# Optimization experiments

Measured on AMD Instinct MI355X. Metric: run time of the kernel, lower is better.

## Reference

```python
import jax, jax.numpy as jnp
import numpy as np

N = 50000   # nodes
E = 640000  # edges
D = 128     # feature dim (din == dmid, required since edge_attr is reused every layer)
L = 5       # GINEConv layers
BN_EPS = 1e-5


def setup_inputs() -> dict:
    key = jax.random.key(0)
    ks = jax.random.split(key, 8)
    x = jax.random.normal(ks[0], (N, D), dtype=jnp.float32)
    edge_index = jax.random.randint(ks[1], (2, E), 0, N, dtype=jnp.int64)
    edge_attr = jax.random.normal(ks[2], (E, D), dtype=jnp.float32)
    W1 = jax.random.normal(ks[3], (L, D, D), dtype=jnp.float32) * 0.05
    b1 = jnp.zeros((L, D), dtype=jnp.float32)
    gamma = jnp.ones((L, D), dtype=jnp.float32)
    beta = jnp.zeros((L, D), dtype=jnp.float32)
    W2 = jax.random.normal(ks[4], (L, D, D), dtype=jnp.float32) * 0.05
    b2 = jnp.zeros((L, D), dtype=jnp.float32)
    return {"x": x, "edge_index": edge_index, "edge_attr": edge_attr,
            "W1": W1, "b1": b1, "gamma": gamma, "beta": beta, "W2": W2, "b2": b2}


def reference(x, edge_index, edge_attr, W1, b1, gamma, beta, W2, b2):
    src, dst = edge_index[0], edge_index[1]  # PyG: messages flow src(j) -> dst(i)
    h = x
    for l in range(L):
        # GINEConv message + aggregate: sum_j ReLU(x_j + e_ij)
        m = jax.nn.relu(h[src] + edge_attr)               # [E, D] gather + add
        agg = jax.ops.segment_sum(m, dst, num_segments=N)  # [N, D] scatter-sum
        h = agg + h  # (1 + eps) * x_i with eps = 0
        # MLP: Linear -> BatchNorm1d (batch stats) -> ReLU -> Linear
        h = h @ W1[l] + b1[l]
        mu = jnp.mean(h, axis=0)
        var = jnp.var(h, axis=0)  # biased var, as torch BN uses for normalization
        h = gamma[l] * (h - mu) * jax.lax.rsqrt(var + BN_EPS) + beta[l]
        h = jax.nn.relu(h)
        h = h @ W2[l] + b2[l]
    return h
```

## Files before the change

kernel.cpp:

```cpp
#include <hip/hip_runtime.h>
#include <hip/hip_bf16.h>
#include <stdint.h>

#define D 128
#define LAYERS 5
#define BN_EPS 1e-5f

typedef unsigned int uint32;
typedef __bf16 bf16x8 __attribute__((ext_vector_type(8)));
typedef float f32x4 __attribute__((ext_vector_type(4)));
typedef float f32x2 __attribute__((ext_vector_type(2)));

__device__ inline unsigned short f2bf(float f) {
    uint32 u = __float_as_uint(f);
    return (unsigned short)((u + 0x7fffu + ((u >> 16) & 1u)) >> 16);
}
__device__ inline float bflo(uint32 p) { return __uint_as_float(p << 16); }
__device__ inline float bfhi(uint32 p) { return __uint_as_float(p & 0xffff0000u); }
__device__ inline uint32 pack2(float a, float b) {
    return (uint32)f2bf(a) | ((uint32)f2bf(b) << 16);
}


__global__ void detect_kernel(const int* __restrict__ ei, int* __restrict__ flag) {
    if (threadIdx.x == 0 && blockIdx.x == 0) {
        int allz = 1;
#pragma unroll
        for (int i = 0; i < 16; ++i) allz &= (ei[2 * i + 1] == 0);
        *flag = allz;
    }
}


__global__ __launch_bounds__(256) void hist_kernel(const int* __restrict__ ei,
                                                   const int* __restrict__ flag,
                                                   int* __restrict__ deg, int E, int n) {
    int e = blockIdx.x * blockDim.x + threadIdx.x;
    if (e >= E) return;
    int is64 = *flag;
    int d = is64 ? ei[2 * ((size_t)E + e)] : ei[E + e];
    if ((unsigned)d < (unsigned)n) atomicAdd(&deg[d], 1);
}

__global__ __launch_bounds__(1024) void scan_kernel(const int* __restrict__ deg,
                                                    int* __restrict__ off, int n) {
    __shared__ int tsum[1024];
    int t = threadIdx.x;
    int CH = (n + 1023) >> 10;
    int lo = t * CH;
    int hi = lo + CH; if (hi > n) hi = n;
    int s = 0;
    for (int i = lo; i < hi; ++i) s += deg[i];
    tsum[t] = s;
    __syncthreads();
    for (int d = 1; d < 1024; d <<= 1) {
        int v = (t >= d) ? tsum[t - d] : 0;
        __syncthreads();
        tsum[t] += v;
        __syncthreads();
    }
    int run = tsum[t] - s;
    for (int i = lo; i < hi; ++i) { off[i] = run; run += deg[i]; }
    if (t == 1023) off[n] = tsum[1023];
}

__global__ __launch_bounds__(256) void fill_kernel(const int* __restrict__ ei,
                                                   const int* __restrict__ flag,
                                                   const int* __restrict__ off,
                                                   int* __restrict__ cursor,
                                                   int* __restrict__ srcs,
                                                   int* __restrict__ eidx, int E, int n) {
    int e = blockIdx.x * blockDim.x + threadIdx.x;
    if (e >= E) return;
    int is64 = *flag;
    int d = is64 ? ei[2 * ((size_t)E + e)] : ei[E + e];
    int s = is64 ? ei[2 * (size_t)e] : ei[e];
    if ((unsigned)d >= (unsigned)n || (unsigned)s >= (unsigned)n) return;
    int p = atomicAdd(&cursor[d], 1);
    int pos = off[d] + p;
    srcs[pos] = s;
    eidx[pos] = e;
}


__global__ __launch_bounds__(256) void wt_kernel(const float* __restrict__ W1,
                                                 const float* __restrict__ W2,
                                                 unsigned short* __restrict__ wt) {
    int id = blockIdx.x * 256 + threadIdx.x;
    if (id >= 10 * 16384) return;
    int l = id >> 14;
    int rem = id & 16383;
    int nn = rem >> 7, kk = rem & 127;
    const float* base = (l < 5) ? (W1 + (size_t)l * 16384) : (W2 + (size_t)(l - 5) * 16384);
    wt[(size_t)l * 16384 + nn * 128 + kk] = f2bf(base[kk * 128 + nn]);
}


__global__ __launch_bounds__(256) void xb_kernel(const float* __restrict__ x,
                                                 uint32* __restrict__ xb, int total) {
    int i = blockIdx.x * 256 + threadIdx.x;
    if (i >= total) return;
    f32x2 v = *(const f32x2*)(x + 2 * (size_t)i);
    xb[i] = pack2(v.x, v.y);
}


__global__ __launch_bounds__(256) void cvt_kernel(const float* __restrict__ ea,
                                                  const int* __restrict__ eidx,
                                                  uint32* __restrict__ eab, int E) {
    int wid = ((blockIdx.x * 256 + threadIdx.x) >> 6) * 2;
    int lane = threadIdx.x & 63;
    if (wid >= E) return;
    int y0 = eidx[wid];
    f32x2 v0 = __builtin_nontemporal_load((const f32x2*)(ea + (size_t)y0 * D + lane * 2));
    if (wid + 1 < E) {
        int y1 = eidx[wid + 1];
        f32x2 v1 = __builtin_nontemporal_load((const f32x2*)(ea + (size_t)y1 * D + lane * 2));
        __builtin_nontemporal_store(pack2(v0.x, v0.y), eab + (size_t)wid * 64 + lane);
        __builtin_nontemporal_store(pack2(v1.x, v1.y), eab + (size_t)(wid + 1) * 64 + lane);
    } else {
        __builtin_nontemporal_store(pack2(v0.x, v0.y), eab + (size_t)wid * 64 + lane);
    }
}


__global__ __launch_bounds__(256) void agg_kernel(const uint32* __restrict__ h,
                                                  const uint32* __restrict__ eab,
                                                  const int* __restrict__ off,
                                                  const int* __restrict__ srcs,
                                                  uint32* __restrict__ out, int n) {
    int node = blockIdx.x * 4 + (threadIdx.x >> 6);
    if (node >= n) return;
    int lane = threadIdx.x & 63;
    uint32 hn = h[(size_t)node * 64 + lane];
    float2 acc = make_float2(bflo(hn), bfhi(hn));
    int e = off[node], end = off[node + 1];
    for (; e + 4 <= end; e += 4) {
        int s0 = srcs[e], s1 = srcs[e + 1], s2 = srcs[e + 2], s3 = srcs[e + 3];
        uint32 a0 = __builtin_nontemporal_load(eab + (size_t)e * 64 + lane);
        uint32 a1 = __builtin_nontemporal_load(eab + (size_t)(e + 1) * 64 + lane);
        uint32 a2 = __builtin_nontemporal_load(eab + (size_t)(e + 2) * 64 + lane);
        uint32 a3 = __builtin_nontemporal_load(eab + (size_t)(e + 3) * 64 + lane);
        uint32 h0 = h[(size_t)s0 * 64 + lane];
        uint32 h1 = h[(size_t)s1 * 64 + lane];
        uint32 h2 = h[(size_t)s2 * 64 + lane];
        uint32 h3 = h[(size_t)s3 * 64 + lane];
        acc.x += fmaxf(bflo(h0) + bflo(a0), 0.f) + fmaxf(bflo(h1) + bflo(a1), 0.f)
               + fmaxf(bflo(h2) + bflo(a2), 0.f) + fmaxf(bflo(h3) + bflo(a3), 0.f);
        acc.y += fmaxf(bfhi(h0) + bfhi(a0), 0.f) + fmaxf(bfhi(h1) + bfhi(a1), 0.f)
               + fmaxf(bfhi(h2) + bfhi(a2), 0.f) + fmaxf(bfhi(h3) + bfhi(a3), 0.f);
    }
    for (; e < end; ++e) {
        int s0 = srcs[e];
        uint32 a0 = eab[(size_t)e * 64 + lane];
        uint32 h0 = h[(size_t)s0 * 64 + lane];
        acc.x += fmaxf(bflo(h0) + bflo(a0), 0.f);
        acc.y += fmaxf(bfhi(h0) + bfhi(a0), 0.f);
    }
    out[(size_t)node * 64 + lane] = pack2(acc.x, acc.y);
}


template <int MODE, bool F32OUT>
__global__ __launch_bounds__(256) void gemm_kernel(const uint4* __restrict__ A,
                                                   const uint4* __restrict__ Wt4,
                                                   const float* __restrict__ bias,
                                                   void* __restrict__ outp,
                                                   float* __restrict__ colstats,
                                                   const float* __restrict__ gamma,
                                                   const float* __restrict__ beta,
                                                   float inv_n, int n) {
    __shared__ float red[256];
    const int t = threadIdx.x;
    const int wv = t >> 6, l = t & 63;
    const int lrow = l & 15, lk = l >> 4;
    const int r0 = blockIdx.x * 64 + wv * 16;

    if (MODE == 1) {
        red[t] = 0.f;
    } else {
        if (t < 128) {
            float mu = colstats[t] * inv_n;
            float var = colstats[128 + t] * inv_n - mu * mu;
            float inv = rsqrtf(var + BN_EPS);
            float sc = gamma[t] * inv;
            red[t] = sc;
            red[128 + t] = beta[t] - mu * sc;
        }
    }
    __syncthreads();

    bf16x8 af[4];
    const int arow = r0 + lrow;
    const bool rowok = arow < n;
#pragma unroll
    for (int c = 0; c < 4; ++c) {
        union { uint4 u; bf16x8 v; uint32 w[4]; } bu;
        bu.u = make_uint4(0u, 0u, 0u, 0u);
        if (rowok) bu.u = A[(size_t)arow * 16 + c * 4 + lk];
        if (MODE == 2) {
            const int kb = c * 32 + lk * 8;
            float xv[8];
#pragma unroll
            for (int i = 0; i < 4; ++i) {
                xv[2 * i]     = bflo(bu.w[i]);
                xv[2 * i + 1] = bfhi(bu.w[i]);
            }
#pragma unroll
            for (int j = 0; j < 8; ++j)
                xv[j] = fmaxf(fmaf(red[kb + j], xv[j], red[128 + kb + j]), 0.f);
#pragma unroll
            for (int i = 0; i < 4; ++i)
                bu.w[i] = pack2(xv[2 * i], xv[2 * i + 1]);
        }
        af[c] = bu.v;
    }

    float* outF = (float*)outp;
    unsigned short* outB = (unsigned short*)outp;
    float s[8], s2[8];

#pragma unroll
    for (int n0 = 0; n0 < 8; ++n0) {
        const int wcol = n0 * 16 + lrow;
        f32x4 acc = {0.f, 0.f, 0.f, 0.f};
#pragma unroll
        for (int c = 0; c < 4; ++c) {
            union { uint4 u; bf16x8 v; } bu;
            bu.u = Wt4[wcol * 16 + c * 4 + lk];
            acc = __builtin_amdgcn_mfma_f32_16x16x32_bf16(af[c], bu.v, acc, 0, 0, 0);
        }
        const float bcol = bias[wcol];
        float ls = 0.f, ls2 = 0.f;
#pragma unroll
        for (int r = 0; r < 4; ++r) {
            int row = r0 + lk * 4 + r;
            float v = acc[r] + bcol;
            if (row < n) {
                if (F32OUT) outF[(size_t)row * D + wcol] = v;
                else        outB[(size_t)row * D + wcol] = f2bf(v);
                if (MODE == 1) { ls += v; ls2 += v * v; }
            }
        }
        s[n0] = ls; s2[n0] = ls2;
    }

    if (MODE == 1) {
#pragma unroll
        for (int n0 = 0; n0 < 8; ++n0) {
            const int wcol = n0 * 16 + lrow;
            float ls = s[n0], ls2 = s2[n0];
            ls  += __shfl_xor(ls, 16);  ls  += __shfl_xor(ls, 32);
            ls2 += __shfl_xor(ls2, 16); ls2 += __shfl_xor(ls2, 32);
            if (lk == 0) {
                atomicAdd(&red[wcol], ls);
                atomicAdd(&red[D + wcol], ls2);
            }
        }
        __syncthreads();
        if (t < 128) {
            atomicAdd(&colstats[t], red[t]);
            atomicAdd(&colstats[D + t], red[D + t]);
        }
    }
}


extern "C" void kernel_launch(void* const* d_in, const int* in_sizes, int n_in,
                              void* d_out, int out_size, void* d_ws, size_t ws_size,
                              hipStream_t stream) {
    const float* x      = (const float*)d_in[0];
    const int*   ei     = (const int*)d_in[1];
    const float* ea     = (const float*)d_in[2];
    const float* W1     = (const float*)d_in[3];
    const float* b1     = (const float*)d_in[4];
    const float* gamma  = (const float*)d_in[5];
    const float* beta   = (const float*)d_in[6];
    const float* W2     = (const float*)d_in[7];
    const float* b2     = (const float*)d_in[8];
    const int N = in_sizes[0] / D;
    const int E = in_sizes[1] / 2;

    char* w = (char*)d_ws;
    auto alloc = [&](size_t bytes) {
        char* p = w;
        w += (bytes + 255) & ~(size_t)255;
        return p;
    };
    int*    off      = (int*)alloc((size_t)(N + 1) * sizeof(int));
    int*    zbase    = (int*)alloc(((size_t)2 * N + 5 * 256) * sizeof(int));
    int*    deg      = zbase;
    int*    cursor   = zbase + N;
    float*  colstats = (float*)(zbase + 2 * N);
    int*    flag     = (int*)alloc(256);
    unsigned short* wt = (unsigned short*)alloc(10 * 16384 * sizeof(unsigned short));
    int*    srcs     = (int*)alloc((size_t)E * sizeof(int));
    int*    eidx     = (int*)alloc((size_t)E * sizeof(int));
    uint32* eab      = (uint32*)alloc((size_t)E * 64 * sizeof(uint32));
    uint32* xb       = (uint32*)alloc((size_t)N * 64 * sizeof(uint32));
    uint32* G        = (uint32*)alloc((size_t)N * 64 * sizeof(uint32));
    uint32* T        = (uint32*)alloc((size_t)N * 64 * sizeof(uint32));
    uint32* H        = (uint32*)alloc((size_t)N * 64 * sizeof(uint32));

    wt_kernel<<<(10 * 16384 + 255) / 256, 256, 0, stream>>>(W1, W2, wt);
    detect_kernel<<<1, 64, 0, stream>>>(ei, flag);
    hipMemsetAsync(zbase, 0, ((size_t)2 * N + 5 * 256) * sizeof(int), stream);
    hist_kernel<<<(E + 255) / 256, 256, 0, stream>>>(ei, flag, deg, E, N);
    scan_kernel<<<1, 1024, 0, stream>>>(deg, off, N);
    fill_kernel<<<(E + 255) / 256, 256, 0, stream>>>(ei, flag, off, cursor, srcs, eidx, E, N);
    xb_kernel<<<(N * 64 + 255) / 256, 256, 0, stream>>>(x, xb, N * 64);
    cvt_kernel<<<(E + 7) / 8, 256, 0, stream>>>(ea, eidx, eab, E);

    const int gemmBlocks = (N + 63) / 64;
    const int aggBlocks  = (N + 3) / 4;
    const float inv_n = 1.0f / (float)N;

    const uint32* hin = xb;
    for (int l = 0; l < LAYERS; ++l) {
        float* cst = colstats + l * 256;
        const uint4* wt1 = (const uint4*)(wt + (size_t)l * 16384);
        const uint4* wt2 = (const uint4*)(wt + (size_t)(5 + l) * 16384);
        agg_kernel<<<aggBlocks, 256, 0, stream>>>(hin, eab, off, srcs, G, N);
        gemm_kernel<1, false><<<gemmBlocks, 256, 0, stream>>>(
            (const uint4*)G, wt1, b1 + l * D, T, cst, nullptr, nullptr, inv_n, N);
        if (l < LAYERS - 1)
            gemm_kernel<2, false><<<gemmBlocks, 256, 0, stream>>>(
                (const uint4*)T, wt2, b2 + l * D, H, cst,
                gamma + l * D, beta + l * D, inv_n, N);
        else
            gemm_kernel<2, true><<<gemmBlocks, 256, 0, stream>>>(
                (const uint4*)T, wt2, b2 + l * D, d_out, cst,
                gamma + l * D, beta + l * D, inv_n, N);
        hin = H;
    }
}
```

Measured before the change: 849.3 us.

## Fuse edge-attr conversion into first-layer aggregation and vectorize gather loads

New measurement: 782.8 us. 1.08x faster.

```diff
diff --git a/kernel.cpp b/kernel.cpp
--- a/kernel.cpp
+++ b/kernel.cpp
@@ -10,6 +10,8 @@
 typedef __bf16 bf16x8 __attribute__((ext_vector_type(8)));
 typedef float f32x4 __attribute__((ext_vector_type(4)));
 typedef float f32x2 __attribute__((ext_vector_type(2)));
+typedef uint32 u32x2 __attribute__((ext_vector_type(2)));
+typedef uint32 u32x4 __attribute__((ext_vector_type(4)));
 
 __device__ inline unsigned short f2bf(float f) {
     uint32 u = __float_as_uint(f);
@@ -96,30 +98,54 @@
 }
 
 
-__global__ __launch_bounds__(256) void xb_kernel(const float* __restrict__ x,
-                                                 uint32* __restrict__ xb, int total) {
-    int i = blockIdx.x * 256 + threadIdx.x;
-    if (i >= total) return;
-    f32x2 v = *(const f32x2*)(x + 2 * (size_t)i);
-    xb[i] = pack2(v.x, v.y);
-}
-
-
-__global__ __launch_bounds__(256) void cvt_kernel(const float* __restrict__ ea,
-                                                  const int* __restrict__ eidx,
-                                                  uint32* __restrict__ eab, int E) {
-    int wid = ((blockIdx.x * 256 + threadIdx.x) >> 6) * 2;
-    int lane = threadIdx.x & 63;
-    if (wid >= E) return;
-    int y0 = eidx[wid];
-    f32x2 v0 = __builtin_nontemporal_load((const f32x2*)(ea + (size_t)y0 * D + lane * 2));
-    if (wid + 1 < E) {
-        int y1 = eidx[wid + 1];
-        f32x2 v1 = __builtin_nontemporal_load((const f32x2*)(ea + (size_t)y1 * D + lane * 2));
-        __builtin_nontemporal_store(pack2(v0.x, v0.y), eab + (size_t)wid * 64 + lane);
-        __builtin_nontemporal_store(pack2(v1.x, v1.y), eab + (size_t)(wid + 1) * 64 + lane);
-    } else {
-        __builtin_nontemporal_store(pack2(v0.x, v0.y), eab + (size_t)wid * 64 + lane);
+__global__ __launch_bounds__(256) void agg_cvt_kernel(const float* __restrict__ x,
+                                                      const float* __restrict__ ea,
+                                                      const int* __restrict__ off,
+                                                      const int* __restrict__ srcs,
+                                                      const int* __restrict__ eidx,
+                                                      uint32* __restrict__ eab,
+                                                      uint32* __restrict__ out, int n) {
+    int node = blockIdx.x * 4 + (threadIdx.x >> 6);
+    if (node >= n) return;
+    const int lane = threadIdx.x & 63;
+    const int half = lane >> 5;
+    const int q = lane & 31;
+    f32x4 acc = {0.f, 0.f, 0.f, 0.f};
+    int e = off[node], end = off[node + 1];
+    for (; e + 4 <= end; e += 4) {
+        int eA = e + half, eB = e + 2 + half;
+        int sA = srcs[eA], sB = srcs[eB];
+        int yA = eidx[eA], yB = eidx[eB];
+        f32x4 va = __builtin_nontemporal_load((const f32x4*)(ea + (size_t)yA * D + q * 4));
+        f32x4 vb = __builtin_nontemporal_load((const f32x4*)(ea + (size_t)yB * D + q * 4));
+        f32x4 ha = *(const f32x4*)(x + (size_t)sA * D + q * 4);
+        f32x4 hb = *(const f32x4*)(x + (size_t)sB * D + q * 4);
+#pragma unroll
+        for (int k = 0; k < 4; ++k)
+            acc[k] += fmaxf(ha[k] + va[k], 0.f) + fmaxf(hb[k] + vb[k], 0.f);
+        u32x2 pa = {pack2(va[0], va[1]), pack2(va[2], va[3])};
+        u32x2 pb = {pack2(vb[0], vb[1]), pack2(vb[2], vb[3])};
+        __builtin_nontemporal_store(pa, (u32x2*)(eab + (size_t)eA * 64 + q * 2));
+        __builtin_nontemporal_store(pb, (u32x2*)(eab + (size_t)eB * 64 + q * 2));
+    }
+    for (; e < end; ++e) {
+        if (half == 0) {
+            int s0 = srcs[e], y0 = eidx[e];
+            f32x4 v = __builtin_nontemporal_load((const f32x4*)(ea + (size_t)y0 * D + q * 4));
+            f32x4 h = *(const f32x4*)(x + (size_t)s0 * D + q * 4);
+#pragma unroll
+            for (int k = 0; k < 4; ++k) acc[k] += fmaxf(h[k] + v[k], 0.f);
+            u32x2 pv = {pack2(v[0], v[1]), pack2(v[2], v[3])};
+            __builtin_nontemporal_store(pv, (u32x2*)(eab + (size_t)e * 64 + q * 2));
+        }
+    }
+#pragma unroll
+    for (int k = 0; k < 4; ++k) acc[k] += __shfl_xor(acc[k], 32);
+    if (half == 0) {
+        f32x4 xs = *(const f32x4*)(x + (size_t)node * D + q * 4);
+        u32x2 o = {pack2(xs[0] + acc[0], xs[1] + acc[1]),
+                   pack2(xs[2] + acc[2], xs[3] + acc[3])};
+        *(u32x2*)(out + (size_t)node * 64 + q * 2) = o;
     }
 }
 
@@ -131,33 +157,63 @@
                                                   uint32* __restrict__ out, int n) {
     int node = blockIdx.x * 4 + (threadIdx.x >> 6);
     if (node >= n) return;
-    int lane = threadIdx.x & 63;
-    uint32 hn = h[(size_t)node * 64 + lane];
-    float2 acc = make_float2(bflo(hn), bfhi(hn));
+    const int lane = threadIdx.x & 63;
+    const int g = lane >> 4;
+    const int j = lane & 15;
+    float acc[8] = {0.f, 0.f, 0.f, 0.f, 0.f, 0.f, 0.f, 0.f};
     int e = off[node], end = off[node + 1];
-    for (; e + 4 <= end; e += 4) {
-        int s0 = srcs[e], s1 = srcs[e + 1], s2 = srcs[e + 2], s3 = srcs[e + 3];
-        uint32 a0 = __builtin_nontemporal_load(eab + (size_t)e * 64 + lane);
-        uint32 a1 = __builtin_nontemporal_load(eab + (size_t)(e + 1) * 64 + lane);
-        uint32 a2 = __builtin_nontemporal_load(eab + (size_t)(e + 2) * 64 + lane);
-        uint32 a3 = __builtin_nontemporal_load(eab + (size_t)(e + 3) * 64 + lane);
-        uint32 h0 = h[(size_t)s0 * 64 + lane];
-        uint32 h1 = h[(size_t)s1 * 64 + lane];
-        uint32 h2 = h[(size_t)s2 * 64 + lane];
-        uint32 h3 = h[(size_t)s3 * 64 + lane];
-        acc.x += fmaxf(bflo(h0) + bflo(a0), 0.f) + fmaxf(bflo(h1) + bflo(a1), 0.f)
-               + fmaxf(bflo(h2) + bflo(a2), 0.f) + fmaxf(bflo(h3) + bflo(a3), 0.f);
-        acc.y += fmaxf(bfhi(h0) + bfhi(a0), 0.f) + fmaxf(bfhi(h1) + bfhi(a1), 0.f)
-               + fmaxf(bfhi(h2) + bfhi(a2), 0.f) + fmaxf(bfhi(h3) + bfhi(a3), 0.f);
+    for (; e + 8 <= end; e += 8) {
+        int e0 = e + g, e1 = e + 4 + g;
+        int s0 = srcs[e0], s1 = srcs[e1];
+        u32x4 a0 = __builtin_nontemporal_load((const u32x4*)(eab + (size_t)e0 * 64 + j * 4));
+        u32x4 a1 = __builtin_nontemporal_load((const u32x4*)(eab + (size_t)e1 * 64 + j * 4));
+        u32x4 h0 = *(const u32x4*)(h + (size_t)s0 * 64 + j * 4);
+        u32x4 h1 = *(const u32x4*)(h + (size_t)s1 * 64 + j * 4);
+#pragma unroll
+        for (int k = 0; k < 4; ++k) {
+            acc[2 * k]     += fmaxf(bflo(h0[k]) + bflo(a0[k]), 0.f)
+                            + fmaxf(bflo(h1[k]) + bflo(a1[k]), 0.f);
+            acc[2 * k + 1] += fmaxf(bfhi(h0[k]) + bfhi(a0[k]), 0.f)
+                            + fmaxf(bfhi(h1[k]) + bfhi(a1[k]), 0.f);
+        }
+    }
+    if (e + 4 <= end) {
+        int e0 = e + g;
+        int s0 = srcs[e0];
+        u32x4 a0 = __builtin_nontemporal_load((const u32x4*)(eab + (size_t)e0 * 64 + j * 4));
+        u32x4 h0 = *(const u32x4*)(h + (size_t)s0 * 64 + j * 4);
+#pragma unroll
+        for (int k = 0; k < 4; ++k) {
+            acc[2 * k]     += fmaxf(bflo(h0[k]) + bflo(a0[k]), 0.f);
+            acc[2 * k + 1] += fmaxf(bfhi(h0[k]) + bfhi(a0[k]), 0.f);
+        }
+        e += 4;
     }
     for (; e < end; ++e) {
-        int s0 = srcs[e];
-        uint32 a0 = eab[(size_t)e * 64 + lane];
-        uint32 h0 = h[(size_t)s0 * 64 + lane];
-        acc.x += fmaxf(bflo(h0) + bflo(a0), 0.f);
-        acc.y += fmaxf(bfhi(h0) + bfhi(a0), 0.f);
-    }
-    out[(size_t)node * 64 + lane] = pack2(acc.x, acc.y);
+        if (g == 0) {
+            int s0 = srcs[e];
+            u32x4 a0 = *(const u32x4*)(eab + (size_t)e * 64 + j * 4);
+            u32x4 h0 = *(const u32x4*)(h + (size_t)s0 * 64 + j * 4);
+#pragma unroll
+            for (int k = 0; k < 4; ++k) {
+                acc[2 * k]     += fmaxf(bflo(h0[k]) + bflo(a0[k]), 0.f);
+                acc[2 * k + 1] += fmaxf(bfhi(h0[k]) + bfhi(a0[k]), 0.f);
+            }
+        }
+    }
+#pragma unroll
+    for (int k = 0; k < 8; ++k) {
+        acc[k] += __shfl_xor(acc[k], 16);
+        acc[k] += __shfl_xor(acc[k], 32);
+    }
+    if (g == 0) {
+        u32x4 hn = *(const u32x4*)(h + (size_t)node * 64 + j * 4);
+        u32x4 o;
+#pragma unroll
+        for (int k = 0; k < 4; ++k)
+            o[k] = pack2(bflo(hn[k]) + acc[2 * k], bfhi(hn[k]) + acc[2 * k + 1]);
+        *(u32x4*)(out + (size_t)node * 64 + j * 4) = o;
+    }
 }
 
 
@@ -297,7 +353,6 @@
     int*    srcs     = (int*)alloc((size_t)E * sizeof(int));
     int*    eidx     = (int*)alloc((size_t)E * sizeof(int));
     uint32* eab      = (uint32*)alloc((size_t)E * 64 * sizeof(uint32));
-    uint32* xb       = (uint32*)alloc((size_t)N * 64 * sizeof(uint32));
     uint32* G        = (uint32*)alloc((size_t)N * 64 * sizeof(uint32));
     uint32* T        = (uint32*)alloc((size_t)N * 64 * sizeof(uint32));
     uint32* H        = (uint32*)alloc((size_t)N * 64 * sizeof(uint32));
@@ -308,19 +363,20 @@
     hist_kernel<<<(E + 255) / 256, 256, 0, stream>>>(ei, flag, deg, E, N);
     scan_kernel<<<1, 1024, 0, stream>>>(deg, off, N);
     fill_kernel<<<(E + 255) / 256, 256, 0, stream>>>(ei, flag, off, cursor, srcs, eidx, E, N);
-    xb_kernel<<<(N * 64 + 255) / 256, 256, 0, stream>>>(x, xb, N * 64);
-    cvt_kernel<<<(E + 7) / 8, 256, 0, stream>>>(ea, eidx, eab, E);
 
     const int gemmBlocks = (N + 63) / 64;
     const int aggBlocks  = (N + 3) / 4;
     const float inv_n = 1.0f / (float)N;
 
-    const uint32* hin = xb;
+    const uint32* hin = nullptr;
     for (int l = 0; l < LAYERS; ++l) {
         float* cst = colstats + l * 256;
         const uint4* wt1 = (const uint4*)(wt + (size_t)l * 16384);
         const uint4* wt2 = (const uint4*)(wt + (size_t)(5 + l) * 16384);
-        agg_kernel<<<aggBlocks, 256, 0, stream>>>(hin, eab, off, srcs, G, N);
+        if (l == 0)
+            agg_cvt_kernel<<<aggBlocks, 256, 0, stream>>>(x, ea, off, srcs, eidx, eab, G, N);
+        else
+            agg_kernel<<<aggBlocks, 256, 0, stream>>>(hin, eab, off, srcs, G, N);
         gemm_kernel<1, false><<<gemmBlocks, 256, 0, stream>>>(
             (const uint4*)G, wt1, b1 + l * D, T, cst, nullptr, nullptr, inv_n, N);
         if (l < LAYERS - 1)
```
